# Kernel optimization log

Measured on AMD Instinct MI355X. Metric: run time of the kernel, lower is better.

The kernel has to match this reference:

```python
import jax, jax.numpy as jnp
import numpy as np

N = 100000      # nodes
E = 1600000     # edges (self-loops added in reference, as PyG GATConv does)
DIN = 512
DOUT = 16
H = 8           # heads (both layers)
C1 = 8          # out_channels of gat1
NEG_SLOPE = 0.2


def setup_inputs() -> dict:
    key = jax.random.key(0)
    ks = jax.random.split(key, 12)
    s = 0.05  # small init scale
    return {
        "x": jax.random.normal(ks[0], (N, DIN), jnp.float32),
        "edge_index": jax.random.randint(ks[1], (2, E), 0, N, jnp.int32),
        "W1": jax.random.normal(ks[2], (DIN, H * C1), jnp.float32) * s,
        "att_src1": jax.random.normal(ks[3], (H, C1), jnp.float32) * s,
        "att_dst1": jax.random.normal(ks[4], (H, C1), jnp.float32) * s,
        "bias1": jnp.zeros((H * C1,), jnp.float32),
        "prelu_w": jnp.float32(0.25),
        "W2": jax.random.normal(ks[5], (H * C1, H * DOUT), jnp.float32) * s,
        "att_src2": jax.random.normal(ks[6], (H, DOUT), jnp.float32) * s,
        "att_dst2": jax.random.normal(ks[7], (H, DOUT), jnp.float32) * s,
        "bias2": jnp.zeros((DOUT,), jnp.float32),
    }


def gat_layer(x, src, dst, W, a_src, a_dst, bias, heads, outc, concat):
    """PyG-style GATConv (eval mode, self-loops already in src/dst)."""
    n = x.shape[0]
    h = (x @ W).reshape(n, heads, outc)                 # [N, H, C]
    alpha_s = jnp.sum(h * a_src, axis=-1)               # [N, H]
    alpha_d = jnp.sum(h * a_dst, axis=-1)               # [N, H]
    # per-edge score, softmax grouped by destination node
    e = jax.nn.leaky_relu(alpha_s[src] + alpha_d[dst], NEG_SLOPE)   # [E', H]
    emax = jax.ops.segment_max(e, dst, num_segments=n)              # [N, H]
    ex = jnp.exp(e - emax[dst])
    denom = jax.ops.segment_sum(ex, dst, num_segments=n)            # [N, H]
    alpha = ex / denom[dst]                                         # [E', H]
    # weighted aggregation of source features
    out = jax.ops.segment_sum(h[src] * alpha[..., None], dst, num_segments=n)  # [N, H, C]
    out = out.reshape(n, heads * outc) if concat else out.mean(axis=1)
    return out + bias


def reference(x, edge_index, W1, att_src1, att_dst1, bias1, prelu_w,
              W2, att_src2, att_dst2, bias2):
    # add self-loops (PyG GATConv default add_self_loops=True)
    loops = jnp.arange(N, dtype=edge_index.dtype)
    src = jnp.concatenate([edge_index[0], loops])
    dst = jnp.concatenate([edge_index[1], loops])

    h = gat_layer(x, src, dst, W1, att_src1, att_dst1, bias1, H, C1, True)   # [N, 64]
    h = jnp.where(h >= 0, h, prelu_w * h)                                    # PReLU
    h = gat_layer(h, src, dst, W2, att_src2, att_dst2, bias2, H, DOUT, False)  # [N, DOUT]
    return jax.nn.log_softmax(h, axis=1)
```

## Files before the change

kernel.cpp:

```cpp
#include <hip/hip_runtime.h>
#include <hip/hip_bf16.h>

#define NN 100000
#define EE 1600000
#define ET (EE + NN)
#define NBK 391
#define NBLK 208
#define STAGE_CAP 4096
#define AGG_NS 72
#define AGG_HS 1160

typedef unsigned short ushort_t;
typedef short short8 __attribute__((ext_vector_type(8)));
typedef float f32x4 __attribute__((ext_vector_type(4)));

static __device__ __forceinline__ float b2f(unsigned short u) {
    return __uint_as_float(((unsigned int)u) << 16);
}
static __device__ __forceinline__ unsigned short f2b(float f) {
    unsigned int x = __float_as_uint(f);
    return (unsigned short)((x + 0x7fffu + ((x >> 16) & 1u)) >> 16);
}

static __device__ void gemm1_body(const float* __restrict__ x,
                                  const ushort_t* __restrict__ w1t,
                                  ushort_t* __restrict__ h1,
                                  char* smem_, int row0, int tid) {
    ushort_t (*xs)[136] = (ushort_t (*)[136])smem_;
    const int wid = tid >> 6, lane = tid & 63;
    const int l15 = lane & 15, qq = lane >> 4;
    f32x4 acc[4];
#pragma unroll
    for (int i = 0; i < 4; ++i) acc[i] = (f32x4)0.f;
    for (int kc = 0; kc < 4; ++kc) {
        float4 f[8];
#pragma unroll
        for (int i = 0; i < 8; ++i) {
            int f4i = tid + 256 * i;
            int rr = f4i >> 5;
            int cc = f4i & 31;
            long gr = (long)min(row0 + rr, NN - 1);
            f[i] = *(const float4*)(x + gr * 512 + kc * 128 + cc * 4);
        }
        __syncthreads();
#pragma unroll
        for (int i = 0; i < 8; ++i) {
            int f4i = tid + 256 * i;
            int rr = f4i >> 5, cc = f4i & 31;
            uint2 uu;
            uu.x = ((unsigned)f2b(f[i].y) << 16) | f2b(f[i].x);
            uu.y = ((unsigned)f2b(f[i].w) << 16) | f2b(f[i].z);
            *(uint2*)&xs[rr][cc * 4] = uu;
        }
        __syncthreads();
#pragma unroll
        for (int ks = 0; ks < 4; ++ks) {
            short8 b = *(const short8*)(w1t + (size_t)(wid * 16 + l15) * 512 + kc * 128 + ks * 32 + qq * 8);
#pragma unroll
            for (int mt = 0; mt < 4; ++mt) {
                short8 a = *(const short8*)&xs[mt * 16 + l15][ks * 32 + qq * 8];
                acc[mt] = __builtin_amdgcn_mfma_f32_16x16x32_bf16(a, b, acc[mt], 0, 0, 0);
            }
        }
    }
#pragma unroll
    for (int mt = 0; mt < 4; ++mt) {
        int node = row0 + mt * 16 + qq * 4;
#pragma unroll
        for (int rr = 0; rr < 4; ++rr) {
            if (node + rr < NN)
                h1[(size_t)(node + rr) * 64 + wid * 16 + l15] = f2b(acc[mt][rr]);
        }
    }
}

__global__ __launch_bounds__(256) void kfuse0(const float* __restrict__ W1,
                                              const float* __restrict__ W2,
                                              ushort_t* __restrict__ W1T,
                                              ushort_t* __restrict__ W2T,
                                              const int* __restrict__ ei,
                                              int* __restrict__ bbcnt,
                                              const float* __restrict__ aws2,
                                              const float* __restrict__ awd2,
                                              float* __restrict__ qp) {
    __shared__ int hist[NBK];
    const int t = threadIdx.x;
    if ((int)blockIdx.x < 160) {
        int tid = blockIdx.x * 256 + t;
        if (tid < 32768) {
            int k = tid >> 6, c = tid & 63;
            W1T[c * 512 + k] = f2b(W1[tid]);
        } else if (tid < 40960) {
            int q = tid - 32768;
            int k = q >> 7, c = q & 127;
            W2T[c * 64 + k] = f2b(W2[q]);
        }
    } else if ((int)blockIdx.x < 368) {
        const int blk = blockIdx.x - 160;
        for (int i = t; i < NBK; i += 256) hist[i] = 0;
        __syncthreads();
        const int e0 = blk * 8192;
#pragma unroll
        for (int i = 0; i < 32; ++i) {
            int e = e0 + t + 256 * i;
            if (e < ET) {
                int dst = (e < EE) ? ei[EE + e] : (e - EE);
                atomicAdd(&hist[dst >> 8], 1);
            }
        }
        __syncthreads();
        for (int i = t; i < NBK; i += 256) bbcnt[blk * NBK + i] = hist[i];
    } else {
        for (int e = t; e < 1024; e += 256) {
            int base = (e >= 512) ? (e - 512) : e;
            int h = base >> 6, k = base & 63;
            const float* w = (e >= 512) ? awd2 : aws2;
            float val = 0.f;
#pragma unroll
            for (int c = 0; c < 16; ++c) val += W2[k * 128 + h * 16 + c] * w[h * 16 + c];
            qp[e] = val;
        }
    }
}

__global__ __launch_bounds__(512) void kbscan(int* __restrict__ bbcnt,
                                              int* __restrict__ bbase) {
    __shared__ int tot[512];
    const int t = threadIdx.x;
    int total = 0;
    if (t < NBK) {
        int run = 0;
#pragma unroll 8
        for (int blk = 0; blk < NBLK; ++blk) {
            int idx = blk * NBK + t;
            int v = bbcnt[idx];
            bbcnt[idx] = run;
            run += v;
        }
        total = run;
    }
    tot[t] = total;
    __syncthreads();
    for (int off = 1; off < 512; off <<= 1) {
        int u = (t >= off) ? tot[t - off] : 0;
        __syncthreads();
        tot[t] += u;
        __syncthreads();
    }
    if (t < NBK) bbase[t] = tot[t] - total;
    if (t == 0) bbase[NBK] = ET;
}

__global__ __launch_bounds__(256) void kfuse1(const int* __restrict__ ei,
                                              const int* __restrict__ bbcnt,
                                              const int* __restrict__ bbase,
                                              unsigned* __restrict__ pairs,
                                              const float* __restrict__ x,
                                              const ushort_t* __restrict__ w1t,
                                              ushort_t* __restrict__ h1) {
    __shared__ __align__(16) char smem[17408];
    const int t = threadIdx.x;
    if ((int)blockIdx.x < NBLK) {
        int* cur = (int*)smem;
        const int blk = blockIdx.x;
        for (int i = t; i < NBK; i += 256) cur[i] = bbase[i] + bbcnt[blk * NBK + i];
        __syncthreads();
        const int e0 = blk * 8192;
#pragma unroll
        for (int i = 0; i < 32; ++i) {
            int e = e0 + t + 256 * i;
            if (e < ET) {
                int src, dst;
                if (e < EE) { src = ei[e]; dst = ei[EE + e]; } else { src = dst = e - EE; }
                int pos = atomicAdd(&cur[dst >> 8], 1);
                pairs[pos] = (unsigned)src | ((unsigned)(dst & 255) << 17);
            }
        }
    } else {
        gemm1_body(x, w1t, h1, smem, (blockIdx.x - NBLK) * 64, t);
    }
}

__global__ __launch_bounds__(256) void kfuse2(const int* __restrict__ bbase,
                                              const unsigned* __restrict__ pairs,
                                              int* __restrict__ rowp,
                                              int* __restrict__ srt,
                                              const float* __restrict__ x,
                                              const ushort_t* __restrict__ w1t,
                                              ushort_t* __restrict__ h1) {
    __shared__ __align__(16) char smem[19456];
    const int t = threadIdx.x;
    if ((int)blockIdx.x < NBK) {
        int* hist = (int*)smem;
        int* scn = hist + 256;
        int* cur = scn + 256;
        unsigned* stage = (unsigned*)(smem + 3072);
        const int b = blockIdx.x;
        const int j0 = bbase[b], j1 = bbase[b + 1];
        const int cnt = j1 - j0;
        hist[t] = 0;
        __syncthreads();
        for (int i = t; i < cnt; i += 256) {
            unsigned p = pairs[j0 + i];
            if (i < STAGE_CAP) stage[i] = p;
            atomicAdd(&hist[p >> 17], 1);
        }
        __syncthreads();
        const int h = hist[t];
        scn[t] = h;
        __syncthreads();
        for (int off = 1; off < 256; off <<= 1) {
            int u = (t >= off) ? scn[t - off] : 0;
            __syncthreads();
            scn[t] += u;
            __syncthreads();
        }
        const int pref = scn[t] - h;
        const int node = b * 256 + t;
        if (node < NN) rowp[node] = j0 + pref;
        if (b == 0 && t == 0) rowp[NN] = ET;
        cur[t] = pref;
        __syncthreads();
        for (int i = t; i < cnt; i += 256) {
            unsigned p = (i < STAGE_CAP) ? stage[i] : pairs[j0 + i];
            int l = (int)(p >> 17);
            int pos = atomicAdd(&cur[l], 1);
            srt[j0 + pos] = (int)(p & 0x1FFFFu);
        }
    } else {
        gemm1_body(x, w1t, h1, smem, (782 + (int)blockIdx.x - NBK) * 64, t);
    }
}

__global__ __launch_bounds__(256) void kagg1(const int* __restrict__ rowp,
                                             const int* __restrict__ srt,
                                             const ushort_t* __restrict__ h1,
                                             const float* __restrict__ aws,
                                             const float* __restrict__ awd,
                                             const float* __restrict__ b1,
                                             const float* __restrict__ pw,
                                             ushort_t* __restrict__ hin) {
    int tid = blockIdx.x * 256 + threadIdx.x;
    int n = tid >> 4;
    int sub = tid & 15;
    int h = sub >> 1, half = sub & 1;
    float as_w[8], ad_w[8];
#pragma unroll
    for (int c = 0; c < 8; ++c) { as_w[c] = aws[h * 8 + c]; ad_w[c] = awd[h * 8 + c]; }
    uint4 hd = *(const uint4*)(h1 + (size_t)n * 64 + h * 8);
    const ushort_t* hdp = (const ushort_t*)&hd;
    float ad = 0.f;
#pragma unroll
    for (int c = 0; c < 8; ++c) ad += b2f(hdp[c]) * ad_w[c];
    int j0 = rowp[n], j1 = rowp[n + 1];
    float num[8]; float den = 0.f;
#pragma unroll
    for (int c = 0; c < 8; ++c) num[c] = 0.f;
    int j = j0 + half;
    uint4 hv;
    if (j < j1) {
        int s = srt[j];
        hv = *(const uint4*)(h1 + (size_t)s * 64 + h * 8);
    }
    while (j < j1) {
        int jn = j + 2;
        uint4 hn;
        if (jn < j1) {
            int sn = srt[jn];
            hn = *(const uint4*)(h1 + (size_t)sn * 64 + h * 8);
        }
        const ushort_t* hp = (const ushort_t*)&hv;
        float va[8];
#pragma unroll
        for (int c = 0; c < 8; ++c) va[c] = b2f(hp[c]);
        float sc = ad;
#pragma unroll
        for (int c = 0; c < 8; ++c) sc += va[c] * as_w[c];
        sc = (sc >= 0.f) ? sc : 0.2f * sc;
        float w = __expf(sc);
        den += w;
#pragma unroll
        for (int c = 0; c < 8; ++c) num[c] += w * va[c];
        j = jn;
        hv = hn;
    }
#pragma unroll
    for (int c = 0; c < 8; ++c) num[c] += __shfl_xor(num[c], 1);
    den += __shfl_xor(den, 1);
    if (half == 0) {
        float inv = 1.f / den;
        float pwf = pw[0];
        ushort_t o[8];
#pragma unroll
        for (int c = 0; c < 8; ++c) {
            float v = num[c] * inv + b1[h * 8 + c];
            v = (v >= 0.f) ? v : pwf * v;
            o[c] = f2b(v);
        }
        *(uint4*)(hin + (size_t)n * 64 + h * 8) = *(uint4*)o;
    }
}

__global__ __launch_bounds__(256) void kalpha2f(const ushort_t* __restrict__ hin,
                                                const float* __restrict__ qp,
                                                float* __restrict__ as2,
                                                float* __restrict__ ad2) {
    __shared__ float lq[1024];
    const int t = threadIdx.x;
    for (int i = t; i < 1024; i += 256) lq[i] = qp[i];
    __syncthreads();
    int gid = blockIdx.x * 256 + t;
    int n = gid >> 3, h = gid & 7;
    float s = 0.f, d = 0.f;
#pragma unroll
    for (int g = 0; g < 8; ++g) {
        uint4 v = *(const uint4*)(hin + (size_t)n * 64 + g * 8);
        const ushort_t* p = (const ushort_t*)&v;
        float4 qa = *(const float4*)&lq[h * 64 + g * 8];
        float4 qb = *(const float4*)&lq[h * 64 + g * 8 + 4];
        float4 pa = *(const float4*)&lq[512 + h * 64 + g * 8];
        float4 pb = *(const float4*)&lq[512 + h * 64 + g * 8 + 4];
        s += b2f(p[0]) * qa.x + b2f(p[1]) * qa.y + b2f(p[2]) * qa.z + b2f(p[3]) * qa.w;
        s += b2f(p[4]) * qb.x + b2f(p[5]) * qb.y + b2f(p[6]) * qb.z + b2f(p[7]) * qb.w;
        d += b2f(p[0]) * pa.x + b2f(p[1]) * pa.y + b2f(p[2]) * pa.z + b2f(p[3]) * pa.w;
        d += b2f(p[4]) * pb.x + b2f(p[5]) * pb.y + b2f(p[6]) * pb.z + b2f(p[7]) * pb.w;
    }
    as2[gid] = s;
    ad2[gid] = d;
}

__global__ __launch_bounds__(256) void kagg2f(const int* __restrict__ rowp,
                                              const int* __restrict__ srt,
                                              const ushort_t* __restrict__ hin,
                                              const float* __restrict__ as2,
                                              const float* __restrict__ ad2,
                                              const ushort_t* __restrict__ w2t,
                                              const float* __restrict__ b2,
                                              float* __restrict__ out) {
    __shared__ __align__(16) ushort_t agg[8 * AGG_HS];
    __shared__ float red[4][16][16];
    const int t = threadIdx.x;
    const int nl = t >> 4, sub = t & 15;
    const int h = sub >> 1, half = sub & 1;
    const int n = blockIdx.x * 16 + nl;
    const float ad = ad2[n * 8 + h];
    const int j0 = rowp[n], j1 = rowp[n + 1];
    float num[32];
#pragma unroll
    for (int c = 0; c < 32; ++c) num[c] = 0.f;
    float den = 0.f;
    int j = j0;
    int s0 = srt[j];
    float as_ = as2[s0 * 8 + h];
    const ushort_t* rp = hin + (size_t)s0 * 64 + half * 32;
    uint4 r0 = *(const uint4*)(rp);
    uint4 r1 = *(const uint4*)(rp + 8);
    uint4 r2 = *(const uint4*)(rp + 16);
    uint4 r3 = *(const uint4*)(rp + 24);
    while (j < j1) {
        int jn = j + 1;
        uint4 n0, n1, n2, n3;
        float asn = 0.f;
        if (jn < j1) {
            int sn = srt[jn];
            asn = as2[sn * 8 + h];
            const ushort_t* np = hin + (size_t)sn * 64 + half * 32;
            n0 = *(const uint4*)(np);
            n1 = *(const uint4*)(np + 8);
            n2 = *(const uint4*)(np + 16);
            n3 = *(const uint4*)(np + 24);
        }
        float sc = as_ + ad;
        sc = (sc >= 0.f) ? sc : 0.2f * sc;
        float w = __expf(sc);
        den += w;
        {
            const ushort_t* p = (const ushort_t*)&r0;
#pragma unroll
            for (int c = 0; c < 8; ++c) num[c] += w * b2f(p[c]);
        }
        {
            const ushort_t* p = (const ushort_t*)&r1;
#pragma unroll
            for (int c = 0; c < 8; ++c) num[8 + c] += w * b2f(p[c]);
        }
        {
            const ushort_t* p = (const ushort_t*)&r2;
#pragma unroll
            for (int c = 0; c < 8; ++c) num[16 + c] += w * b2f(p[c]);
        }
        {
            const ushort_t* p = (const ushort_t*)&r3;
#pragma unroll
            for (int c = 0; c < 8; ++c) num[24 + c] += w * b2f(p[c]);
        }
        j = jn;
        r0 = n0; r1 = n1; r2 = n2; r3 = n3;
        as_ = asn;
    }
    float g = 0.125f / den;
#pragma unroll
    for (int q = 0; q < 4; ++q) {
        ushort_t o[8];
#pragma unroll
        for (int c = 0; c < 8; ++c) o[c] = f2b(num[q * 8 + c] * g);
        *(uint4*)&agg[h * AGG_HS + nl * AGG_NS + half * 32 + q * 8] = *(uint4*)o;
    }
    __syncthreads();
    const int wid = t >> 6, lane = t & 63;
    const int l15 = lane & 15, qq = lane >> 4;
    f32x4 acc = (f32x4)0.f;
#pragma unroll
    for (int hh2 = 0; hh2 < 2; ++hh2) {
        int hh = wid + hh2 * 4;
#pragma unroll
        for (int ks = 0; ks < 2; ++ks) {
            short8 a = *(const short8*)&agg[hh * AGG_HS + l15 * AGG_NS + ks * 32 + qq * 8];
            short8 b = *(const short8*)(w2t + (size_t)(hh * 16 + l15) * 64 + ks * 32 + qq * 8);
            acc = __builtin_amdgcn_mfma_f32_16x16x32_bf16(a, b, acc, 0, 0, 0);
        }
    }
#pragma unroll
    for (int r = 0; r < 4; ++r) red[wid][qq * 4 + r][l15] = acc[r];
    __syncthreads();
    {
        int c = sub;
        float v = red[0][nl][c] + red[1][nl][c] + red[2][nl][c] + red[3][nl][c] + b2[c];
        float m = v;
#pragma unroll
        for (int mask = 1; mask <= 8; mask <<= 1) m = fmaxf(m, __shfl_xor(m, mask));
        float e = __expf(v - m);
        float sum = e;
#pragma unroll
        for (int mask = 1; mask <= 8; mask <<= 1) sum += __shfl_xor(sum, mask);
        out[(size_t)n * 16 + c] = v - (__logf(sum) + m);
    }
}

extern "C" void kernel_launch(void* const* d_in, const int* in_sizes, int n_in,
                              void* d_out, int out_size, void* d_ws, size_t ws_size,
                              hipStream_t stream) {
    const float* x    = (const float*)d_in[0];
    const int*   ei   = (const int*)d_in[1];
    const float* W1   = (const float*)d_in[2];
    const float* aws1 = (const float*)d_in[3];
    const float* awd1 = (const float*)d_in[4];
    const float* b1   = (const float*)d_in[5];
    const float* pw   = (const float*)d_in[6];
    const float* W2   = (const float*)d_in[7];
    const float* aws2 = (const float*)d_in[8];
    const float* awd2 = (const float*)d_in[9];
    const float* b2   = (const float*)d_in[10];
    float* out = (float*)d_out;

    char* ws = (char*)d_ws;
    int*      srt   = (int*)(ws + 0);
    int*      rowp  = (int*)(ws + 6800000);
    int*      bbcnt = (int*)(ws + 7200256);
    int*      bbase = (int*)(ws + 7600384);
    unsigned* pairs = (unsigned*)(ws + 8000000);
    ushort_t* hin   = (ushort_t*)(ws + 8000000);
    ushort_t* h1    = (ushort_t*)(ws + 20800000);
    float*    as2   = (float*)(ws + 20800000);
    float*    ad2   = (float*)(ws + 24000000);
    ushort_t* W1T   = (ushort_t*)(ws + 46400000);
    ushort_t* W2T   = (ushort_t*)(ws + 46465536);
    float*    qp    = (float*)(ws + 46481920);

    kfuse0<<<369, 256, 0, stream>>>(W1, W2, W1T, W2T, ei, bbcnt, aws2, awd2, qp);
    kbscan<<<1, 512, 0, stream>>>(bbcnt, bbase);
    kfuse1<<<NBLK + 782, 256, 0, stream>>>(ei, bbcnt, bbase, pairs, x, W1T, h1);
    kfuse2<<<NBK + 781, 256, 0, stream>>>(bbase, pairs, rowp, srt, x, W1T, h1);
    kagg1<<<6250, 256, 0, stream>>>(rowp, srt, h1, aws1, awd1, b1, pw, hin);
    kalpha2f<<<3125, 256, 0, stream>>>(hin, qp, as2, ad2);
    kagg2f<<<6250, 256, 0, stream>>>(rowp, srt, hin, as2, ad2, W2T, b2, out);
}
```

Baseline: 576.8 us.

## Split edge lists four ways per node in both GAT aggregation kernels

```diff
diff --git a/kernel.cpp b/kernel.cpp
--- a/kernel.cpp
+++ b/kernel.cpp
@@ -7,8 +7,7 @@
 #define NBK 391
 #define NBLK 208
 #define STAGE_CAP 4096
-#define AGG_NS 72
-#define AGG_HS 1160
+#define AGG_S 584
 
 typedef unsigned short ushort_t;
 typedef short short8 __attribute__((ext_vector_type(8)));
@@ -241,9 +240,9 @@
                                              const float* __restrict__ pw,
                                              ushort_t* __restrict__ hin) {
     int tid = blockIdx.x * 256 + threadIdx.x;
-    int n = tid >> 4;
-    int sub = tid & 15;
-    int h = sub >> 1, half = sub & 1;
+    int n = tid >> 5;
+    int sub = tid & 31;
+    int h = sub & 7, par = sub >> 3;
     float as_w[8], ad_w[8];
 #pragma unroll
     for (int c = 0; c < 8; ++c) { as_w[c] = aws[h * 8 + c]; ad_w[c] = awd[h * 8 + c]; }
@@ -256,14 +255,14 @@
     float num[8]; float den = 0.f;
 #pragma unroll
     for (int c = 0; c < 8; ++c) num[c] = 0.f;
-    int j = j0 + half;
+    int j = j0 + par;
     uint4 hv;
     if (j < j1) {
         int s = srt[j];
         hv = *(const uint4*)(h1 + (size_t)s * 64 + h * 8);
     }
     while (j < j1) {
-        int jn = j + 2;
+        int jn = j + 4;
         uint4 hn;
         if (jn < j1) {
             int sn = srt[jn];
@@ -285,9 +284,12 @@
         hv = hn;
     }
 #pragma unroll
-    for (int c = 0; c < 8; ++c) num[c] += __shfl_xor(num[c], 1);
-    den += __shfl_xor(den, 1);
-    if (half == 0) {
+    for (int c = 0; c < 8; ++c) num[c] += __shfl_xor(num[c], 8);
+    den += __shfl_xor(den, 8);
+#pragma unroll
+    for (int c = 0; c < 8; ++c) num[c] += __shfl_xor(num[c], 16);
+    den += __shfl_xor(den, 16);
+    if (par == 0) {
         float inv = 1.f / den;
         float pwf = pw[0];
         ushort_t o[8];
@@ -329,19 +331,20 @@
     ad2[gid] = d;
 }
 
-__global__ __launch_bounds__(256) void kagg2f(const int* __restrict__ rowp,
-                                              const int* __restrict__ srt,
-                                              const ushort_t* __restrict__ hin,
-                                              const float* __restrict__ as2,
-                                              const float* __restrict__ ad2,
-                                              const ushort_t* __restrict__ w2t,
-                                              const float* __restrict__ b2,
-                                              float* __restrict__ out) {
-    __shared__ __align__(16) ushort_t agg[8 * AGG_HS];
+__global__ __launch_bounds__(1024) void kagg2g(const int* __restrict__ rowp,
+                                               const int* __restrict__ srt,
+                                               const ushort_t* __restrict__ hin,
+                                               const float* __restrict__ as2,
+                                               const float* __restrict__ ad2,
+                                               const ushort_t* __restrict__ w2t,
+                                               const float* __restrict__ b2,
+                                               float* __restrict__ out) {
+    __shared__ __align__(16) ushort_t agg[16][AGG_S];
     __shared__ float red[4][16][16];
     const int t = threadIdx.x;
-    const int nl = t >> 4, sub = t & 15;
-    const int h = sub >> 1, half = sub & 1;
+    const int nl = t >> 6;
+    const int ln = t & 63;
+    const int chh = ln >> 5, par = (ln >> 3) & 3, h = ln & 7;
     const int n = blockIdx.x * 16 + nl;
     const float ad = ad2[n * 8 + h];
     const int j0 = rowp[n], j1 = rowp[n + 1];
@@ -349,26 +352,22 @@
 #pragma unroll
     for (int c = 0; c < 32; ++c) num[c] = 0.f;
     float den = 0.f;
-    int j = j0;
-    int s0 = srt[j];
-    float as_ = as2[s0 * 8 + h];
-    const ushort_t* rp = hin + (size_t)s0 * 64 + half * 32;
-    uint4 r0 = *(const uint4*)(rp);
-    uint4 r1 = *(const uint4*)(rp + 8);
-    uint4 r2 = *(const uint4*)(rp + 16);
-    uint4 r3 = *(const uint4*)(rp + 24);
+    int j = j0 + par;
+    uint4 r0, r1; float as_ = 0.f;
+    if (j < j1) {
+        int s = srt[j];
+        as_ = as2[s * 8 + h];
+        const uint4* rp = (const uint4*)(hin + (size_t)s * 64 + chh * 32);
+        r0 = rp[0]; r1 = rp[1];
+    }
     while (j < j1) {
-        int jn = j + 1;
-        uint4 n0, n1, n2, n3;
-        float asn = 0.f;
+        int jn = j + 4;
+        uint4 n0, n1; float asn = 0.f;
         if (jn < j1) {
             int sn = srt[jn];
             asn = as2[sn * 8 + h];
-            const ushort_t* np = hin + (size_t)sn * 64 + half * 32;
-            n0 = *(const uint4*)(np);
-            n1 = *(const uint4*)(np + 8);
-            n2 = *(const uint4*)(np + 16);
-            n3 = *(const uint4*)(np + 24);
+            const uint4* rp = (const uint4*)(hin + (size_t)sn * 64 + chh * 32);
+            n0 = rp[0]; n1 = rp[1];
         }
         float sc = as_ + ad;
         sc = (sc >= 0.f) ? sc : 0.2f * sc;
@@ -385,47 +384,65 @@
             for (int c = 0; c < 8; ++c) num[8 + c] += w * b2f(p[c]);
         }
         {
-            const ushort_t* p = (const ushort_t*)&r2;
-#pragma unroll
-            for (int c = 0; c < 8; ++c) num[16 + c] += w * b2f(p[c]);
-        }
-        {
-            const ushort_t* p = (const ushort_t*)&r3;
-#pragma unroll
-            for (int c = 0; c < 8; ++c) num[24 + c] += w * b2f(p[c]);
+            const uint4* rp = (const uint4*)(hin + (size_t)srt[j] * 64 + chh * 32);
+            uint4 r2 = rp[2], r3 = rp[3];
+            const ushort_t* p2 = (const ushort_t*)&r2;
+            const ushort_t* p3 = (const ushort_t*)&r3;
+#pragma unroll
+            for (int c = 0; c < 8; ++c) { num[16 + c] += w * b2f(p2[c]); num[24 + c] += w * b2f(p3[c]); }
         }
         j = jn;
-        r0 = n0; r1 = n1; r2 = n2; r3 = n3;
+        r0 = n0; r1 = n1;
         as_ = asn;
     }
-    float g = 0.125f / den;
-#pragma unroll
-    for (int q = 0; q < 4; ++q) {
-        ushort_t o[8];
-#pragma unroll
-        for (int c = 0; c < 8; ++c) o[c] = f2b(num[q * 8 + c] * g);
-        *(uint4*)&agg[h * AGG_HS + nl * AGG_NS + half * 32 + q * 8] = *(uint4*)o;
+#pragma unroll
+    for (int c = 0; c < 32; ++c) num[c] += __shfl_xor(num[c], 8);
+    den += __shfl_xor(den, 8);
+#pragma unroll
+    for (int c = 0; c < 32; ++c) num[c] += __shfl_xor(num[c], 16);
+    den += __shfl_xor(den, 16);
+    if (par == 0) {
+        float g = 0.125f / den;
+#pragma unroll
+        for (int q = 0; q < 4; ++q) {
+            ushort_t o[8];
+#pragma unroll
+            for (int c = 0; c < 8; ++c) o[c] = f2b(num[q * 8 + c] * g);
+            *(uint4*)&agg[nl][h * 72 + chh * 32 * 0 + 0] = *(uint4*)o;
+        }
+    }
+    if (par == 0) {
+        float g = 0.125f / den;
+#pragma unroll
+        for (int q = 0; q < 4; ++q) {
+            int k = (q < 2) ? (chh * 32 + q * 8) : (chh * 32 + (q - 2) * 8 + 16);
+            ushort_t o[8];
+#pragma unroll
+            for (int c = 0; c < 8; ++c) o[c] = f2b(num[q * 8 + c] * g);
+            *(uint4*)&agg[nl][h * 72 + k] = *(uint4*)o;
+        }
     }
     __syncthreads();
-    const int wid = t >> 6, lane = t & 63;
-    const int l15 = lane & 15, qq = lane >> 4;
-    f32x4 acc = (f32x4)0.f;
-#pragma unroll
-    for (int hh2 = 0; hh2 < 2; ++hh2) {
-        int hh = wid + hh2 * 4;
-#pragma unroll
-        for (int ks = 0; ks < 2; ++ks) {
-            short8 a = *(const short8*)&agg[hh * AGG_HS + l15 * AGG_NS + ks * 32 + qq * 8];
-            short8 b = *(const short8*)(w2t + (size_t)(hh * 16 + l15) * 64 + ks * 32 + qq * 8);
-            acc = __builtin_amdgcn_mfma_f32_16x16x32_bf16(a, b, acc, 0, 0, 0);
-        }
-    }
-#pragma unroll
-    for (int r = 0; r < 4; ++r) red[wid][qq * 4 + r][l15] = acc[r];
+    if (t < 256) {
+        const int wid = t >> 6, lane = t & 63, l15 = lane & 15, qq = lane >> 4;
+        f32x4 acc = (f32x4)0.f;
+#pragma unroll
+        for (int hh2 = 0; hh2 < 2; ++hh2) {
+            int hh = wid * 2 + hh2;
+#pragma unroll
+            for (int ks = 0; ks < 2; ++ks) {
+                short8 a = *(const short8*)&agg[l15][hh * 72 + ks * 32 + qq * 8];
+                short8 b = *(const short8*)(w2t + (size_t)(hh * 16 + l15) * 64 + ks * 32 + qq * 8);
+                acc = __builtin_amdgcn_mfma_f32_16x16x32_bf16(a, b, acc, 0, 0, 0);
+            }
+        }
+#pragma unroll
+        for (int r = 0; r < 4; ++r) red[wid][qq * 4 + r][l15] = acc[r];
+    }
     __syncthreads();
-    {
-        int c = sub;
-        float v = red[0][nl][c] + red[1][nl][c] + red[2][nl][c] + red[3][nl][c] + b2[c];
+    if (t < 256) {
+        int node = t >> 4, c = t & 15;
+        float v = red[0][node][c] + red[1][node][c] + red[2][node][c] + red[3][node][c] + b2[c];
         float m = v;
 #pragma unroll
         for (int mask = 1; mask <= 8; mask <<= 1) m = fmaxf(m, __shfl_xor(m, mask));
@@ -433,7 +450,7 @@
         float sum = e;
 #pragma unroll
         for (int mask = 1; mask <= 8; mask <<= 1) sum += __shfl_xor(sum, mask);
-        out[(size_t)n * 16 + c] = v - (__logf(sum) + m);
+        out[(size_t)(blockIdx.x * 16 + node) * 16 + c] = v - (__logf(sum) + m);
     }
 }
 
@@ -471,7 +488,7 @@
     kbscan<<<1, 512, 0, stream>>>(bbcnt, bbase);
     kfuse1<<<NBLK + 782, 256, 0, stream>>>(ei, bbcnt, bbase, pairs, x, W1T, h1);
     kfuse2<<<NBK + 781, 256, 0, stream>>>(bbase, pairs, rowp, srt, x, W1T, h1);
-    kagg1<<<6250, 256, 0, stream>>>(rowp, srt, h1, aws1, awd1, b1, pw, hin);
+    kagg1<<<12500, 256, 0, stream>>>(rowp, srt, h1, aws1, awd1, b1, pw, hin);
     kalpha2f<<<3125, 256, 0, stream>>>(hin, qp, as2, ad2);
-    kagg2f<<<6250, 256, 0, stream>>>(rowp, srt, hin, as2, ad2, W2T, b2, out);
-}
+    kagg2g<<<6250, 1024, 0, stream>>>(rowp, srt, hin, as2, ad2, W2T, b2, out);
+}
```

After: 675.0 us. 1.17x slower.
